# Performance work log

Hardware: AMD Instinct MI355X
Metric: run time of the kernel (lower is better)

The kernel has to match this reference:

```python
import jax, jax.numpy as jnp
import numpy as np

# Model dims (from init_kwargs + mamba_ssm defaults)
D_MODEL = 1024
N_LAYER = 2
D_STATE = 16
D_CONV = 4
D_INNER = 2 * D_MODEL          # expand=2
DT_RANK = D_MODEL // 16        # 64
VOCAB = 32000
BATCH, SEQLEN = 2, 1024


def setup_inputs() -> dict:
    key = jax.random.key(0)
    ks = jax.random.split(key, 10)
    s = 0.02
    x = jax.random.randint(ks[0], (BATCH, SEQLEN), 0, VOCAB)
    embedding = jax.random.normal(ks[1], (VOCAB, D_MODEL), dtype=jnp.float32) * s
    norm_w = jnp.ones((N_LAYER, D_MODEL), dtype=jnp.float32)
    in_proj_w = jax.random.normal(ks[2], (N_LAYER, 2 * D_INNER, D_MODEL), dtype=jnp.float32) * s
    conv_w = jax.random.normal(ks[3], (N_LAYER, D_INNER, D_CONV), dtype=jnp.float32) * (1.0 / np.sqrt(D_CONV))
    conv_b = jnp.zeros((N_LAYER, D_INNER), dtype=jnp.float32)
    x_proj_w = jax.random.normal(ks[4], (N_LAYER, DT_RANK + 2 * D_STATE, D_INNER), dtype=jnp.float32) * s
    dt_proj_w = jax.random.normal(ks[5], (N_LAYER, D_INNER, DT_RANK), dtype=jnp.float32) * (DT_RANK ** -0.5)
    # inverse-softplus of dt_init ~ 0.01 (mamba default dt range)
    dt_bias = jnp.full((N_LAYER, D_INNER), float(np.log(np.expm1(0.01))), dtype=jnp.float32)
    A_log = jnp.log(jnp.broadcast_to(jnp.arange(1, D_STATE + 1, dtype=jnp.float32), (N_LAYER, D_INNER, D_STATE)))
    D = jnp.ones((N_LAYER, D_INNER), dtype=jnp.float32)
    out_proj_w = jax.random.normal(ks[6], (N_LAYER, D_MODEL, D_INNER), dtype=jnp.float32) * s
    final_norm_w = jnp.ones((D_MODEL,), dtype=jnp.float32)
    return {"x": x, "embedding": embedding, "norm_w": norm_w, "in_proj_w": in_proj_w,
            "conv_w": conv_w, "conv_b": conv_b, "x_proj_w": x_proj_w, "dt_proj_w": dt_proj_w,
            "dt_bias": dt_bias, "A_log": A_log, "D": D, "out_proj_w": out_proj_w,
            "final_norm_w": final_norm_w}


def _rmsnorm(h, w, eps=1e-5):
    return h * jax.lax.rsqrt(jnp.mean(h * h, axis=-1, keepdims=True) + eps) * w


def _scan_combine(c1, c2):
    a1, b1 = c1
    a2, b2 = c2
    return a2 * a1, a2 * b1 + b2


def _mamba_block(h, norm_w, in_proj_w, conv_w, conv_b, x_proj_w, dt_proj_w, dt_bias, A_log, D, out_proj_w):
    u = _rmsnorm(h, norm_w)
    xz = jnp.einsum('bld,ed->ble', u, in_proj_w)           # [B,L,2*D_INNER]
    xi, z = jnp.split(xz, 2, axis=-1)
    # depthwise causal conv1d, kernel D_CONV
    k = conv_w.T[:, None, :]                               # [D_CONV, 1, D_INNER]
    xc = jax.lax.conv_general_dilated(xi, k, (1,), [(D_CONV - 1, 0)],
                                      dimension_numbers=('NLC', 'LIO', 'NLC'),
                                      feature_group_count=D_INNER) + conv_b
    xc = jax.nn.silu(xc)
    dbl = jnp.einsum('bld,ed->ble', xc, x_proj_w)          # [B,L,DT_RANK+2*D_STATE]
    dt_low = dbl[..., :DT_RANK]
    Bm = dbl[..., DT_RANK:DT_RANK + D_STATE]
    Cm = dbl[..., DT_RANK + D_STATE:]
    dt = jax.nn.softplus(jnp.einsum('blr,dr->bld', dt_low, dt_proj_w) + dt_bias)
    A = -jnp.exp(A_log)                                    # [D_INNER, D_STATE]
    a = jnp.exp(dt[..., None] * A)                         # [B,L,D_INNER,D_STATE]
    b = dt[..., None] * Bm[:, :, None, :] * xc[..., None]  # [B,L,D_INNER,D_STATE]
    hs = jax.lax.associative_scan(_scan_combine, (a, b), axis=1)[1]
    y = jnp.einsum('bldn,bln->bld', hs, Cm) + xc * D
    y = y * jax.nn.silu(z)
    return h + jnp.einsum('bld,md->blm', y, out_proj_w)


def reference(x, embedding, norm_w, in_proj_w, conv_w, conv_b, x_proj_w, dt_proj_w,
              dt_bias, A_log, D, out_proj_w, final_norm_w):
    h = embedding[x]                                       # [B,L,D_MODEL]
    for i in range(N_LAYER):
        h = _mamba_block(h, norm_w[i], in_proj_w[i], conv_w[i], conv_b[i], x_proj_w[i],
                         dt_proj_w[i], dt_bias[i], A_log[i], D[i], out_proj_w[i])
    h = _rmsnorm(h, final_norm_w)
    logits = jnp.einsum('bld,vd->blv', h, embedding)       # tied lm head
    return logits
```

## Files before the change

### kernel.cpp

```cpp
#include <hip/hip_runtime.h>
#include <hip/hip_bf16.h>
#include <math.h>

#define D_MODEL 1024
#define N_LAYER 2
#define D_STATE 16
#define D_CONV  4
#define D_INNER 2048
#define DT_RANK 64
#define VOCAB   32000
#define BATCH   2
#define SEQLEN  1024
#define TOKENS  (BATCH*SEQLEN)
#define NC      32
#define CL      32

typedef __hip_bfloat16 bf16;
typedef __bf16 bf16x8 __attribute__((ext_vector_type(8)));
typedef float f32x4 __attribute__((ext_vector_type(4)));

__device__ inline void gld_lds16(const bf16* g, bf16* l) {
    __builtin_amdgcn_global_load_lds(
        (const __attribute__((address_space(1))) void*)g,
        (__attribute__((address_space(3))) void*)l, 16, 0, 0);
}

__device__ inline float softplus_fast(float v) {
    return (v > 20.f) ? v : __logf(1.f + __expf(v));
}
__device__ inline float silu_fast(float v) {
    return v / (1.f + __expf(-v));
}

__global__ __launch_bounds__(256) void embed_kernel(const int* __restrict__ x,
                                                    const float* __restrict__ emb,
                                                    float* __restrict__ h) {
    int t = blockIdx.x;
    int tok = x[t];
    const float4* src = (const float4*)(emb + (size_t)tok * D_MODEL);
    float4* dst = (float4*)(h + (size_t)t * D_MODEL);
    dst[threadIdx.x] = src[threadIdx.x];
}

__global__ __launch_bounds__(256) void rmsnorm_bf16(const float* __restrict__ h,
                                                    const float* __restrict__ w,
                                                    bf16* __restrict__ u) {
    int t = blockIdx.x;
    const float4* hv = (const float4*)(h + (size_t)t * D_MODEL);
    float4 v = hv[threadIdx.x];
    float ss = v.x*v.x + v.y*v.y + v.z*v.z + v.w*v.w;
    #pragma unroll
    for (int off = 32; off > 0; off >>= 1) ss += __shfl_down(ss, off);
    __shared__ float red[4];
    int lane = threadIdx.x & 63, wid = threadIdx.x >> 6;
    if (lane == 0) red[wid] = ss;
    __syncthreads();
    float tot = red[0] + red[1] + red[2] + red[3];
    float scale = rsqrtf(tot * (1.0f / (float)D_MODEL) + 1e-5f);
    float4 wq = ((const float4*)w)[threadIdx.x];
    size_t o = (size_t)t * D_MODEL + threadIdx.x * 4;
    u[o+0] = __float2bfloat16(v.x * scale * wq.x);
    u[o+1] = __float2bfloat16(v.y * scale * wq.y);
    u[o+2] = __float2bfloat16(v.z * scale * wq.z);
    u[o+3] = __float2bfloat16(v.w * scale * wq.w);
}

__global__ __launch_bounds__(256) void f32_to_bf16(const float* __restrict__ s,
                                                   bf16* __restrict__ d, int n) {
    int i = (blockIdx.x * 256 + threadIdx.x) * 4;
    if (i < n) {
        float4 v = *(const float4*)(s + i);
        d[i+0] = __float2bfloat16(v.x);
        d[i+1] = __float2bfloat16(v.y);
        d[i+2] = __float2bfloat16(v.z);
        d[i+3] = __float2bfloat16(v.w);
    }
}

__global__ __launch_bounds__(256) void conv_xproj_pad(const float* __restrict__ s,
                                                      bf16* __restrict__ d) {
    int col = blockIdx.x * 256 + threadIdx.x;
    int row = blockIdx.y;
    int layer = blockIdx.z;
    float v = (row < 96) ? s[((size_t)layer * 96 + row) * D_INNER + col] : 0.f;
    d[((size_t)layer * 128 + row) * D_INNER + col] = __float2bfloat16(v);
}

__global__ __launch_bounds__(256) void gemm_bf16(
    const bf16* __restrict__ A, int lda,
    const bf16* __restrict__ W, int ldw,
    float* __restrict__ C, int ldc,
    int N, int K, int acc, int swz, int M, int bfout)
{
    __shared__ bf16 lds[2][2][128 * 64];
    int bx = blockIdx.x, by = blockIdx.y;
    if (swz) {
        int bid = by * gridDim.x + bx;
        int q = (gridDim.x * gridDim.y) >> 3;
        int n = (bid & 7) * q + (bid >> 3);
        by = n % gridDim.y;
        bx = n / gridDim.y;
    }
    const int z = blockIdx.z;
    A += (size_t)z * K;
    W += (size_t)z * K;
    C += (size_t)z * M * (size_t)ldc;

    const int tid  = threadIdx.x;
    const int wave = tid >> 6;
    const int lane = tid & 63;
    const int wr = wave >> 1, wc = wave & 1;
    const size_t rowBase = (size_t)by * 128;
    const size_t colBase = (size_t)bx * 128;

    const int srow = 8 * wave + (lane >> 3);
    const int scol = ((lane & 7) ^ (lane >> 3)) << 3;
    const bf16* aGs = A + (rowBase + srow) * (size_t)lda + scol;
    const bf16* bGs = W + (colBase + srow) * (size_t)ldw + scol;

#define STAGE(tt, bb) do {                                                      \
        const size_t kofs_ = (size_t)(tt) * 64;                                 \
        _Pragma("unroll")                                                       \
        for (int i_ = 0; i_ < 4; ++i_) {                                        \
            gld_lds16(aGs + kofs_ + (size_t)(32 * i_) * lda,                    \
                      &lds[bb][0][(32 * i_ + 8 * wave) * 64]);                  \
            gld_lds16(bGs + kofs_ + (size_t)(32 * i_) * ldw,                    \
                      &lds[bb][1][(32 * i_ + 8 * wave) * 64]);                  \
        }                                                                       \
    } while (0)

    f32x4 accv[4][4];
    #pragma unroll
    for (int i = 0; i < 4; ++i)
        #pragma unroll
        for (int j = 0; j < 4; ++j)
            accv[i][j] = f32x4{0.f, 0.f, 0.f, 0.f};

    const int arow0 = wr * 64 + (lane & 15);
    const int brow0 = wc * 64 + (lane & 15);
    const int h8  = (lane >> 4) << 3;
    const int sw8 = (lane & 7) << 3;

    const int NT = K >> 6;
    STAGE(0, 0);
    for (int t = 0; t < NT; ++t) {
        const int cur = t & 1;
        if (t + 1 < NT) {
            STAGE(t + 1, cur ^ 1);
            asm volatile("s_waitcnt vmcnt(8)" ::: "memory");
        } else {
            asm volatile("s_waitcnt vmcnt(0)" ::: "memory");
        }
        __builtin_amdgcn_s_barrier();

        const bf16* Ab = &lds[cur][0][0];
        const bf16* Bb = &lds[cur][1][0];
        #pragma unroll
        for (int kk = 0; kk < 2; ++kk) {
            const int cs = ((kk << 5) + h8) ^ sw8;
            bf16x8 af[4], bv[4];
            #pragma unroll
            for (int i = 0; i < 4; ++i)
                af[i] = *(const bf16x8*)(Ab + (arow0 + 16 * i) * 64 + cs);
            #pragma unroll
            for (int j = 0; j < 4; ++j)
                bv[j] = *(const bf16x8*)(Bb + (brow0 + 16 * j) * 64 + cs);
            #pragma unroll
            for (int i = 0; i < 4; ++i)
                #pragma unroll
                for (int j = 0; j < 4; ++j)
                    accv[i][j] = __builtin_amdgcn_mfma_f32_16x16x32_bf16(
                        af[i], bv[j], accv[i][j], 0, 0, 0);
        }
        asm volatile("s_waitcnt lgkmcnt(0)" ::: "memory");
        __builtin_amdgcn_s_barrier();
    }
#undef STAGE

    const int cl = lane & 15;
    const int rg = (lane >> 4) * 4;
    #pragma unroll
    for (int i = 0; i < 4; ++i) {
        #pragma unroll
        for (int j = 0; j < 4; ++j) {
            int col = (int)colBase + wc * 64 + j * 16 + cl;
            if (col < N) {
                size_t base = (rowBase + wr * 64 + i * 16 + rg) * (size_t)ldc + col;
                if (bfout) {
                    bf16* Cb = (bf16*)C;
                    #pragma unroll
                    for (int r = 0; r < 4; ++r)
                        Cb[base + (size_t)r * ldc] = __float2bfloat16(accv[i][j][r]);
                } else {
                    #pragma unroll
                    for (int r = 0; r < 4; ++r) {
                        size_t idx = base + (size_t)r * ldc;
                        C[idx] = acc ? C[idx] + accv[i][j][r] : accv[i][j][r];
                    }
                }
            }
        }
    }
}

__global__ __launch_bounds__(512) void gemm_wide3(
    const bf16* __restrict__ A,
    const bf16* __restrict__ W,
    float* __restrict__ C, int ldc, int bfout)
{
    __shared__ bf16 ldsA[3][256 * 32];
    __shared__ bf16 ldsB[3][128 * 32];
    int bx = blockIdx.x, by = blockIdx.y;
    {
        int bid = by * gridDim.x + bx;
        int n = (bid & 7) * ((gridDim.x * gridDim.y) >> 3) + (bid >> 3);
        by = n & 7;
        bx = n >> 3;
    }
    const int tid  = threadIdx.x;
    const int wave = tid >> 6;
    const int lane = tid & 63;
    const int wr = wave >> 1;
    const int wc = wave & 1;
    const size_t rowBase = (size_t)by * 256;
    const size_t colBase = (size_t)bx * 128;

    const int srow   = lane >> 2;
    const int schunk = ((lane & 3) ^ ((lane >> 3) & 3)) << 3;
    const bf16* aG0 = A + (rowBase + 16 * wave       + srow) * (size_t)D_MODEL + schunk;
    const bf16* aG1 = A + (rowBase + 128 + 16 * wave + srow) * (size_t)D_MODEL + schunk;
    const bf16* bG  = W + (colBase + 16 * wave       + srow) * (size_t)D_MODEL + schunk;

#define STAGEW(tt, sAp, sBp) do {                                               \
        const size_t ko_ = (size_t)(tt) * 32;                                   \
        gld_lds16(aG0 + ko_, (sAp) + 512 * wave);                               \
        gld_lds16(aG1 + ko_, (sAp) + 512 * (8 + wave));                         \
        gld_lds16(bG  + ko_, (sBp) + 512 * wave);                               \
    } while (0)

    f32x4 accv[4][4];
    #pragma unroll
    for (int i = 0; i < 4; ++i)
        #pragma unroll
        for (int j = 0; j < 4; ++j)
            accv[i][j] = f32x4{0.f, 0.f, 0.f, 0.f};

    const int l15 = lane & 15;
    const int cs = (((lane >> 4) ^ ((l15 >> 1) & 3)) << 3);
    const int arow0 = wr * 64 + l15;
    const int brow0 = wc * 64 + l15;

    STAGEW(0, &ldsA[0][0], &ldsB[0][0]);
    STAGEW(1, &ldsA[1][0], &ldsB[1][0]);

    int rs = 0, ps = 2;
    #pragma unroll 1
    for (int t = 0; t < 32; ++t) {
        if (t < 31) { asm volatile("s_waitcnt vmcnt(3)" ::: "memory"); }
        else        { asm volatile("s_waitcnt vmcnt(0)" ::: "memory"); }
        __builtin_amdgcn_s_barrier();
        __builtin_amdgcn_sched_barrier(0);

        if (t + 2 < 32) STAGEW(t + 2, &ldsA[ps][0], &ldsB[ps][0]);

        const bf16* Ab = &ldsA[rs][0];
        const bf16* Bb = &ldsB[rs][0];
        bf16x8 af[4], bv[4];
        #pragma unroll
        for (int i = 0; i < 4; ++i)
            af[i] = *(const bf16x8*)(Ab + (arow0 + 16 * i) * 32 + cs);
        #pragma unroll
        for (int j = 0; j < 4; ++j)
            bv[j] = *(const bf16x8*)(Bb + (brow0 + 16 * j) * 32 + cs);
        #pragma unroll
        for (int i = 0; i < 4; ++i)
            #pragma unroll
            for (int j = 0; j < 4; ++j)
                accv[i][j] = __builtin_amdgcn_mfma_f32_16x16x32_bf16(
                    af[i], bv[j], accv[i][j], 0, 0, 0);

        rs = (rs == 2) ? 0 : rs + 1;
        ps = (ps == 2) ? 0 : ps + 1;
    }
#undef STAGEW

    const int cl = l15;
    const int rg = (lane >> 4) * 4;
    #pragma unroll
    for (int i = 0; i < 4; ++i) {
        #pragma unroll
        for (int j = 0; j < 4; ++j) {
            int col = (int)colBase + wc * 64 + j * 16 + cl;
            size_t base = (rowBase + wr * 64 + i * 16 + rg) * (size_t)ldc + col;
            if (bfout) {
                bf16* Cb = (bf16*)C;
                #pragma unroll
                for (int r = 0; r < 4; ++r)
                    Cb[base + (size_t)r * ldc] = __float2bfloat16(accv[i][j][r]);
            } else {
                #pragma unroll
                for (int r = 0; r < 4; ++r)
                    C[base + (size_t)r * ldc] = accv[i][j][r];
            }
        }
    }
}

__global__ __launch_bounds__(256) void conv_silu_kernel(const bf16* __restrict__ xz,
                                                        const float* __restrict__ cw,
                                                        const float* __restrict__ cb,
                                                        bf16* __restrict__ xcb) {
    int d = blockIdx.x * 256 + threadIdx.x;
    int l0 = blockIdx.y * 8;
    int b = blockIdx.z;
    float w0 = cw[d*4+0], w1 = cw[d*4+1], w2 = cw[d*4+2], w3 = cw[d*4+3];
    float bias = cb[d];
    float win0 = (l0 >= 3) ? __bfloat162float(xz[((size_t)b * SEQLEN + l0 - 3) * (2*D_INNER) + d]) : 0.f;
    float win1 = (l0 >= 2) ? __bfloat162float(xz[((size_t)b * SEQLEN + l0 - 2) * (2*D_INNER) + d]) : 0.f;
    float win2 = (l0 >= 1) ? __bfloat162float(xz[((size_t)b * SEQLEN + l0 - 1) * (2*D_INNER) + d]) : 0.f;
    #pragma unroll
    for (int i = 0; i < 8; ++i) {
        float cur = __bfloat162float(xz[((size_t)b * SEQLEN + l0 + i) * (2*D_INNER) + d]);
        float acc = bias + w0*win0 + w1*win1 + w2*win2 + w3*cur;
        float s = silu_fast(acc);
        xcb[((size_t)b * SEQLEN + l0 + i) * D_INNER + d] = __float2bfloat16(s);
        win0 = win1; win1 = win2; win2 = cur;
    }
}

__global__ __launch_bounds__(256) void reduce_xproj(const float* __restrict__ px,
                                                    float* __restrict__ dblf,
                                                    bf16* __restrict__ dbl_b) {
    int i = blockIdx.x * 256 + threadIdx.x;
    float s = 0.f;
    #pragma unroll
    for (int z = 0; z < 8; ++z) s += px[(size_t)z * (TOKENS*96) + i];
    dblf[i] = s;
    dbl_b[i] = __float2bfloat16(s);
}

__global__ __launch_bounds__(256) void reduce_oproj(const float* __restrict__ po,
                                                    float* __restrict__ h) {
    int i = (blockIdx.x * 256 + threadIdx.x) * 4;
    float4 a = *(const float4*)(po + i);
    float4 b = *(const float4*)(po + (size_t)TOKENS*D_MODEL + i);
    float4 hv = *(const float4*)(h + i);
    hv.x += a.x + b.x; hv.y += a.y + b.y; hv.z += a.z + b.z; hv.w += a.w + b.w;
    *(float4*)(h + i) = hv;
}

__global__ __launch_bounds__(256) void scan_chunk(const bf16* __restrict__ dtp,
                                                  const float* __restrict__ dt_bias,
                                                  const float* __restrict__ dbl,
                                                  const bf16* __restrict__ xc,
                                                  const float* __restrict__ A_log,
                                                  float* __restrict__ aprod,
                                                  float* __restrict__ sfin) {
    int d = blockIdx.x * 256 + threadIdx.x;
    int c = blockIdx.y;
    int b = blockIdx.z;
    __shared__ float Bs[CL][D_STATE];
    for (int i = threadIdx.x; i < CL * D_STATE; i += 256) {
        int l = i >> 4, n = i & 15;
        Bs[l][n] = dbl[((size_t)b * SEQLEN + c * CL + l) * 96 + DT_RANK + n];
    }
    __syncthreads();
    float A[D_STATE];
    #pragma unroll
    for (int n = 0; n < D_STATE; ++n) A[n] = -__expf(A_log[d * D_STATE + n]);
    float bias = dt_bias[d];
    float st[D_STATE];
    #pragma unroll
    for (int n = 0; n < D_STATE; ++n) st[n] = 0.f;
    float dts = 0.f;
    for (int l = 0; l < CL; ++l) {
        size_t t = (size_t)b * SEQLEN + c * CL + l;
        float dtv = softplus_fast(__bfloat162float(dtp[t * D_INNER + d]) + bias);
        dts += dtv;
        float dx = dtv * __bfloat162float(xc[t * D_INNER + d]);
        #pragma unroll
        for (int n = 0; n < D_STATE; ++n) {
            float a = __expf(dtv * A[n]);
            st[n] = a * st[n] + dx * Bs[l][n];
        }
    }
    #pragma unroll
    for (int n = 0; n < D_STATE; ++n) {
        size_t o = (((size_t)b * NC + c) * D_STATE + n) * D_INNER + d;
        aprod[o] = __expf(dts * A[n]);
        sfin[o] = st[n];
    }
}

__global__ __launch_bounds__(256) void scan_carry(const float* __restrict__ aprod,
                                                  const float* __restrict__ sfin,
                                                  float* __restrict__ initS) {
    int idx = blockIdx.x * 256 + threadIdx.x;
    int d = idx & (D_INNER - 1);
    int n = (idx >> 11) & (D_STATE - 1);
    int b = idx >> 15;
    float st = 0.f;
    for (int c = 0; c < NC; ++c) {
        size_t o = (((size_t)b * NC + c) * D_STATE + n) * D_INNER + d;
        initS[o] = st;
        st = aprod[o] * st + sfin[o];
    }
}

__global__ __launch_bounds__(256) void scan_emit(const bf16* __restrict__ dtp,
                                                 const float* __restrict__ dt_bias,
                                                 const float* __restrict__ dbl,
                                                 const bf16* __restrict__ xc,
                                                 const bf16* __restrict__ xz,
                                                 const float* __restrict__ A_log,
                                                 const float* __restrict__ Dp,
                                                 const float* __restrict__ initS,
                                                 bf16* __restrict__ y) {
    int d = blockIdx.x * 256 + threadIdx.x;
    int c = blockIdx.y;
    int b = blockIdx.z;
    __shared__ float BCs[CL][2 * D_STATE];
    for (int i = threadIdx.x; i < CL * 2 * D_STATE; i += 256) {
        int l = i >> 5, n = i & 31;
        BCs[l][n] = dbl[((size_t)b * SEQLEN + c * CL + l) * 96 + DT_RANK + n];
    }
    __syncthreads();
    float A[D_STATE];
    #pragma unroll
    for (int n = 0; n < D_STATE; ++n) A[n] = -__expf(A_log[d * D_STATE + n]);
    float bias = dt_bias[d];
    float Dv = Dp[d];
    float st[D_STATE];
    #pragma unroll
    for (int n = 0; n < D_STATE; ++n)
        st[n] = initS[(((size_t)b * NC + c) * D_STATE + n) * D_INNER + d];
    for (int l = 0; l < CL; ++l) {
        size_t t = (size_t)b * SEQLEN + c * CL + l;
        float dtv = softplus_fast(__bfloat162float(dtp[t * D_INNER + d]) + bias);
        float xcv = __bfloat162float(xc[t * D_INNER + d]);
        float dx = dtv * xcv;
        float acc = 0.f;
        #pragma unroll
        for (int n = 0; n < D_STATE; ++n) {
            float a = __expf(dtv * A[n]);
            st[n] = a * st[n] + dx * BCs[l][n];
            acc += st[n] * BCs[l][D_STATE + n];
        }
        acc += xcv * Dv;
        float zv = __bfloat162float(xz[t * (2 * D_INNER) + D_INNER + d]);
        y[t * D_INNER + d] = __float2bfloat16(acc * silu_fast(zv));
    }
}

extern "C" void kernel_launch(void* const* d_in, const int* in_sizes, int n_in,
                              void* d_out, int out_size, void* d_ws, size_t ws_size,
                              hipStream_t stream) {
    const int*   x          = (const int*)  d_in[0];
    const float* emb        = (const float*)d_in[1];
    const float* norm_w     = (const float*)d_in[2];
    const float* in_proj_w  = (const float*)d_in[3];
    const float* conv_w     = (const float*)d_in[4];
    const float* conv_b     = (const float*)d_in[5];
    const float* x_proj_w   = (const float*)d_in[6];
    const float* dt_proj_w  = (const float*)d_in[7];
    const float* dt_bias    = (const float*)d_in[8];
    const float* A_log      = (const float*)d_in[9];
    const float* Dp         = (const float*)d_in[10];
    const float* out_proj_w = (const float*)d_in[11];
    const float* fnorm_w    = (const float*)d_in[12];
    float* out = (float*)d_out;
    float* ws  = (float*)d_ws;

    bf16*  embf   = (bf16*)ws;
    bf16*  u_b    = (bf16*)(ws + 16384000);
    bf16*  xz_b   = (bf16*)(ws + 17432576);
    bf16*  dtp_b  = (bf16*)(ws + 25821184);
    bf16*  xc_b   = (bf16*)(ws + 30015488);
    float* h      = ws + 36306944;
    float* dblf   = ws + 38404096;
    bf16*  dbl_b  = (bf16*)(ws + 38600704);
    bf16*  y_b    = (bf16*)(ws + 38699008);
    bf16*  inpj_b = (bf16*)(ws + 40796160);
    bf16*  xpj_b  = (bf16*)(ws + 44990464);
    bf16*  dtpj_b = (bf16*)(ws + 45252608);
    bf16*  otpj_b = (bf16*)(ws + 45383680);
    float* aprod  = ws + 47480832;
    float* sfin   = ws + 49577984;
    float* initS  = ws + 51675136;
    float* px     = ws + 53772288;
    float* po     = ws + 55345152;

    f32_to_bf16<<<(VOCAB*D_MODEL/4 + 255)/256, 256, 0, stream>>>(emb, embf, VOCAB*D_MODEL);
    f32_to_bf16<<<(2*2*D_INNER*D_MODEL/4 + 255)/256, 256, 0, stream>>>(in_proj_w,  inpj_b, 2*2*D_INNER*D_MODEL);
    conv_xproj_pad<<<dim3(D_INNER/256, 128, N_LAYER), 256, 0, stream>>>(x_proj_w, xpj_b);
    f32_to_bf16<<<(2*D_INNER*DT_RANK/4 + 255)/256, 256, 0, stream>>>(dt_proj_w,  dtpj_b, 2*D_INNER*DT_RANK);
    f32_to_bf16<<<(2*D_MODEL*D_INNER/4 + 255)/256, 256, 0, stream>>>(out_proj_w, otpj_b, 2*D_MODEL*D_INNER);

    embed_kernel<<<TOKENS, 256, 0, stream>>>(x, emb, h);

    for (int layer = 0; layer < N_LAYER; ++layer) {
        rmsnorm_bf16<<<TOKENS, 256, 0, stream>>>(h, norm_w + layer * D_MODEL, u_b);
        gemm_wide3<<<dim3(4096/128, TOKENS/256), 512, 0, stream>>>(
            u_b, inpj_b + (size_t)layer * 2 * D_INNER * D_MODEL,
            (float*)xz_b, 2 * D_INNER, 1);
        conv_silu_kernel<<<dim3(D_INNER/256, SEQLEN/8, BATCH), 256, 0, stream>>>(
            xz_b, conv_w + (size_t)layer * D_INNER * D_CONV, conv_b + layer * D_INNER,
            xc_b);
        gemm_bf16<<<dim3(1, TOKENS/128, 8), 256, 0, stream>>>(
            xc_b, D_INNER, xpj_b + (size_t)layer * 128 * D_INNER, D_INNER,
            px, 96, 96, 256, 0, 0, TOKENS, 0);
        reduce_xproj<<<(TOKENS*96)/256, 256, 0, stream>>>(px, dblf, dbl_b);
        gemm_bf16<<<dim3(D_INNER/128, TOKENS/128), 256, 0, stream>>>(
            dbl_b, 96, dtpj_b + (size_t)layer * D_INNER * DT_RANK, DT_RANK,
            (float*)dtp_b, D_INNER, D_INNER, DT_RANK, 0, 1, TOKENS, 1);
        scan_chunk<<<dim3(D_INNER/256, NC, BATCH), 256, 0, stream>>>(
            dtp_b, dt_bias + layer * D_INNER, dblf, xc_b,
            A_log + (size_t)layer * D_INNER * D_STATE, aprod, sfin);
        scan_carry<<<(BATCH*D_STATE*D_INNER)/256, 256, 0, stream>>>(aprod, sfin, initS);
        scan_emit<<<dim3(D_INNER/256, NC, BATCH), 256, 0, stream>>>(
            dtp_b, dt_bias + layer * D_INNER, dblf, xc_b, xz_b,
            A_log + (size_t)layer * D_INNER * D_STATE, Dp + layer * D_INNER,
            initS, y_b);
        gemm_bf16<<<dim3(D_MODEL/128, TOKENS/128, 2), 256, 0, stream>>>(
            y_b, D_INNER, otpj_b + (size_t)layer * D_MODEL * D_INNER, D_INNER,
            po, D_MODEL, D_MODEL, 1024, 0, 1, TOKENS, 0);
        reduce_oproj<<<(TOKENS*D_MODEL/4)/256, 256, 0, stream>>>(po, h);
    }

    rmsnorm_bf16<<<TOKENS, 256, 0, stream>>>(h, fnorm_w, u_b);

    gemm_wide3<<<dim3(VOCAB/128, TOKENS/256), 512, 0, stream>>>(u_b, embf, out, VOCAB, 0);
}
```

Before: 545.5 us.

## Add dedicated 256x128 vocab GEMM and fuse residual reduce with RMSNorm

Replaces the final LM-head GEMM with a specialized kernel that uses 256 threads per 256x128 tile, so each wave owns a 128x64 sub-tile. It uses triple-buffered LDS staging via direct global-to-LDS loads and a grouped block swizzle for L2 reuse of the embedding weights. It also fuses the out-proj partial-sum reduction with the next layer's RMSNorm (or the final norm), which removes separate rmsnorm launches and an extra pass over h. The larger per-wave accumulator tile raises register pressure and may lower occupancy.

```diff
diff --git a/kernel.cpp b/kernel.cpp
--- a/kernel.cpp
+++ b/kernel.cpp
@@ -306,6 +306,104 @@
     }
 }
 
+__global__ __launch_bounds__(256) void gemm_vocab4(
+    const bf16* __restrict__ A,
+    const bf16* __restrict__ W,
+    float* __restrict__ C)
+{
+    __shared__ bf16 ldsA[3][256 * 32];
+    __shared__ bf16 ldsB[3][128 * 32];
+    int bx = blockIdx.x, by = blockIdx.y;
+    {
+        int bid = by * gridDim.x + bx;
+        int n = (bid & 7) * ((gridDim.x * gridDim.y) >> 3) + (bid >> 3);
+        by = n & 7;
+        bx = n >> 3;
+    }
+    const int tid  = threadIdx.x;
+    const int wave = tid >> 6;
+    const int lane = tid & 63;
+    const int wr = wave >> 1;
+    const int wc = wave & 1;
+    const size_t rowBase = (size_t)by * 256;
+    const size_t colBase = (size_t)bx * 128;
+
+    const int srow   = lane >> 2;
+    const int schunk = ((lane & 3) ^ ((lane >> 3) & 3)) << 3;
+    const bf16* aG = A + (rowBase + 64 * wave + srow) * (size_t)D_MODEL + schunk;
+    const bf16* bG = W + (colBase + 32 * wave + srow) * (size_t)D_MODEL + schunk;
+
+#define STGV(tt, sl) do {                                                       \
+        const size_t ko_ = (size_t)(tt) * 32;                                   \
+        gld_lds16(aG + ko_,                          &ldsA[sl][(64*wave     )*32]); \
+        gld_lds16(aG + ko_ + (size_t)16 * D_MODEL,   &ldsA[sl][(64*wave + 16)*32]); \
+        gld_lds16(aG + ko_ + (size_t)32 * D_MODEL,   &ldsA[sl][(64*wave + 32)*32]); \
+        gld_lds16(aG + ko_ + (size_t)48 * D_MODEL,   &ldsA[sl][(64*wave + 48)*32]); \
+        gld_lds16(bG + ko_,                          &ldsB[sl][(32*wave     )*32]); \
+        gld_lds16(bG + ko_ + (size_t)16 * D_MODEL,   &ldsB[sl][(32*wave + 16)*32]); \
+    } while (0)
+
+    f32x4 accv[8][4];
+    #pragma unroll
+    for (int i = 0; i < 8; ++i)
+        #pragma unroll
+        for (int j = 0; j < 4; ++j)
+            accv[i][j] = f32x4{0.f, 0.f, 0.f, 0.f};
+
+    const int l15 = lane & 15;
+    const int cs = (((lane >> 4) ^ ((l15 >> 1) & 3)) << 3);
+    const int arow0 = wr * 128 + l15;
+    const int brow0 = wc * 64 + l15;
+
+    STGV(0, 0);
+    STGV(1, 1);
+
+    int rs = 0, ps = 2;
+    #pragma unroll 1
+    for (int t = 0; t < 32; ++t) {
+        if (t < 31) { asm volatile("s_waitcnt vmcnt(6)" ::: "memory"); }
+        else        { asm volatile("s_waitcnt vmcnt(0)" ::: "memory"); }
+        __builtin_amdgcn_s_barrier();
+        __builtin_amdgcn_sched_barrier(0);
+
+        if (t + 2 < 32) STGV(t + 2, ps);
+
+        const bf16* Ab = &ldsA[rs][0];
+        const bf16* Bb = &ldsB[rs][0];
+        bf16x8 af[8], bv[4];
+        #pragma unroll
+        for (int j = 0; j < 4; ++j)
+            bv[j] = *(const bf16x8*)(Bb + (brow0 + 16 * j) * 32 + cs);
+        #pragma unroll
+        for (int i = 0; i < 8; ++i)
+            af[i] = *(const bf16x8*)(Ab + (arow0 + 16 * i) * 32 + cs);
+        #pragma unroll
+        for (int i = 0; i < 8; ++i)
+            #pragma unroll
+            for (int j = 0; j < 4; ++j)
+                accv[i][j] = __builtin_amdgcn_mfma_f32_16x16x32_bf16(
+                    af[i], bv[j], accv[i][j], 0, 0, 0);
+
+        rs = (rs == 2) ? 0 : rs + 1;
+        ps = (ps == 2) ? 0 : ps + 1;
+    }
+#undef STGV
+
+    const int cl = l15;
+    const int rg = (lane >> 4) * 4;
+    #pragma unroll
+    for (int i = 0; i < 8; ++i) {
+        #pragma unroll
+        for (int j = 0; j < 4; ++j) {
+            int col = (int)colBase + wc * 64 + j * 16 + cl;
+            size_t base = (rowBase + wr * 128 + i * 16 + rg) * (size_t)VOCAB + col;
+            #pragma unroll
+            for (int r = 0; r < 4; ++r)
+                C[base + (size_t)r * VOCAB] = accv[i][j][r];
+        }
+    }
+}
+
 __global__ __launch_bounds__(256) void conv_silu_kernel(const bf16* __restrict__ xz,
                                                         const float* __restrict__ cw,
                                                         const float* __restrict__ cb,
@@ -339,14 +437,31 @@
     dbl_b[i] = __float2bfloat16(s);
 }
 
-__global__ __launch_bounds__(256) void reduce_oproj(const float* __restrict__ po,
-                                                    float* __restrict__ h) {
-    int i = (blockIdx.x * 256 + threadIdx.x) * 4;
-    float4 a = *(const float4*)(po + i);
-    float4 b = *(const float4*)(po + (size_t)TOKENS*D_MODEL + i);
-    float4 hv = *(const float4*)(h + i);
+__global__ __launch_bounds__(256) void reduce_oproj_rms(const float* __restrict__ po,
+                                                        float* __restrict__ h,
+                                                        const float* __restrict__ w,
+                                                        bf16* __restrict__ u) {
+    int t = blockIdx.x;
+    size_t base = (size_t)t * D_MODEL + threadIdx.x * 4;
+    float4 a = *(const float4*)(po + base);
+    float4 b = *(const float4*)(po + (size_t)TOKENS * D_MODEL + base);
+    float4 hv = *(const float4*)(h + base);
     hv.x += a.x + b.x; hv.y += a.y + b.y; hv.z += a.z + b.z; hv.w += a.w + b.w;
-    *(float4*)(h + i) = hv;
+    *(float4*)(h + base) = hv;
+    float ss = hv.x*hv.x + hv.y*hv.y + hv.z*hv.z + hv.w*hv.w;
+    #pragma unroll
+    for (int off = 32; off > 0; off >>= 1) ss += __shfl_down(ss, off);
+    __shared__ float red[4];
+    int lane = threadIdx.x & 63, wid = threadIdx.x >> 6;
+    if (lane == 0) red[wid] = ss;
+    __syncthreads();
+    float tot = red[0] + red[1] + red[2] + red[3];
+    float scale = rsqrtf(tot * (1.0f / (float)D_MODEL) + 1e-5f);
+    float4 wq = ((const float4*)w)[threadIdx.x];
+    u[base+0] = __float2bfloat16(hv.x * scale * wq.x);
+    u[base+1] = __float2bfloat16(hv.y * scale * wq.y);
+    u[base+2] = __float2bfloat16(hv.z * scale * wq.z);
+    u[base+3] = __float2bfloat16(hv.w * scale * wq.w);
 }
 
 __global__ __launch_bounds__(256) void scan_chunk(const bf16* __restrict__ dtp,
@@ -497,9 +612,9 @@
     f32_to_bf16<<<(2*D_MODEL*D_INNER/4 + 255)/256, 256, 0, stream>>>(out_proj_w, otpj_b, 2*D_MODEL*D_INNER);
 
     embed_kernel<<<TOKENS, 256, 0, stream>>>(x, emb, h);
+    rmsnorm_bf16<<<TOKENS, 256, 0, stream>>>(h, norm_w, u_b);
 
     for (int layer = 0; layer < N_LAYER; ++layer) {
-        rmsnorm_bf16<<<TOKENS, 256, 0, stream>>>(h, norm_w + layer * D_MODEL, u_b);
         gemm_wide3<<<dim3(4096/128, TOKENS/256), 512, 0, stream>>>(
             u_b, inpj_b + (size_t)layer * 2 * D_INNER * D_MODEL,
             (float*)xz_b, 2 * D_INNER, 1);
@@ -524,10 +639,10 @@
         gemm_bf16<<<dim3(D_MODEL/128, TOKENS/128, 2), 256, 0, stream>>>(
             y_b, D_INNER, otpj_b + (size_t)layer * D_MODEL * D_INNER, D_INNER,
             po, D_MODEL, D_MODEL, 1024, 0, 1, TOKENS, 0);
-        reduce_oproj<<<(TOKENS*D_MODEL/4)/256, 256, 0, stream>>>(po, h);
-    }
-
-    rmsnorm_bf16<<<TOKENS, 256, 0, stream>>>(h, fnorm_w, u_b);
-
-    gemm_wide3<<<dim3(VOCAB/128, TOKENS/256), 512, 0, stream>>>(u_b, embf, out, VOCAB, 0);
-}
+        reduce_oproj_rms<<<TOKENS, 256, 0, stream>>>(
+            po, h, (layer + 1 < N_LAYER) ? (norm_w + (layer + 1) * D_MODEL) : fnorm_w,
+            u_b);
+    }
+
+    gemm_vocab4<<<dim3(VOCAB/128, TOKENS/256), 256, 0, stream>>>(u_b, embf, out);
+}
```

New measurement: 550.4 us. No clear change (+0.9%).

## Fuse rmsnorm into embed and out-proj reduce, bf16 partials, recompute scan decay

Applied to the files above, without the earlier changes.

Merges the embedding gather with the first RMSNorm, and the out-projection split-K reduction with the next layer's (or the final) RMSNorm. This removes three rmsnorm launches and their re-reads of h. The out-projection split-K partials are now written as bf16 instead of fp32, halving that traffic but rounding the partial sums. The scan's per-chunk decay products are no longer stored per state; only the per-channel dt sum is written and scan_carry recomputes exp(dts*A), cutting memory traffic in exchange for extra exp work.

```diff
diff --git a/kernel.cpp b/kernel.cpp
--- a/kernel.cpp
+++ b/kernel.cpp
@@ -31,23 +31,22 @@
 __device__ inline float silu_fast(float v) {
     return v / (1.f + __expf(-v));
 }
-
-__global__ __launch_bounds__(256) void embed_kernel(const int* __restrict__ x,
-                                                    const float* __restrict__ emb,
-                                                    float* __restrict__ h) {
+__device__ inline float bfu(unsigned short s) {
+    unsigned u = ((unsigned)s) << 16;
+    float f;
+    __builtin_memcpy(&f, &u, 4);
+    return f;
+}
+
+__global__ __launch_bounds__(256) void embed_rms(const int* __restrict__ x,
+                                                 const float* __restrict__ emb,
+                                                 const float* __restrict__ w,
+                                                 float* __restrict__ h,
+                                                 bf16* __restrict__ u) {
     int t = blockIdx.x;
     int tok = x[t];
-    const float4* src = (const float4*)(emb + (size_t)tok * D_MODEL);
-    float4* dst = (float4*)(h + (size_t)t * D_MODEL);
-    dst[threadIdx.x] = src[threadIdx.x];
-}
-
-__global__ __launch_bounds__(256) void rmsnorm_bf16(const float* __restrict__ h,
-                                                    const float* __restrict__ w,
-                                                    bf16* __restrict__ u) {
-    int t = blockIdx.x;
-    const float4* hv = (const float4*)(h + (size_t)t * D_MODEL);
-    float4 v = hv[threadIdx.x];
+    float4 v = ((const float4*)(emb + (size_t)tok * D_MODEL))[threadIdx.x];
+    ((float4*)(h + (size_t)t * D_MODEL))[threadIdx.x] = v;
     float ss = v.x*v.x + v.y*v.y + v.z*v.z + v.w*v.w;
     #pragma unroll
     for (int off = 32; off > 0; off >>= 1) ss += __shfl_down(ss, off);
@@ -104,7 +103,8 @@
     const int z = blockIdx.z;
     A += (size_t)z * K;
     W += (size_t)z * K;
-    C += (size_t)z * M * (size_t)ldc;
+    float* Cf = C + (size_t)z * M * (size_t)ldc;
+    bf16*  Cb = (bf16*)C + (size_t)z * M * (size_t)ldc;
 
     const int tid  = threadIdx.x;
     const int wave = tid >> 6;
@@ -187,7 +187,6 @@
             if (col < N) {
                 size_t base = (rowBase + wr * 64 + i * 16 + rg) * (size_t)ldc + col;
                 if (bfout) {
-                    bf16* Cb = (bf16*)C;
                     #pragma unroll
                     for (int r = 0; r < 4; ++r)
                         Cb[base + (size_t)r * ldc] = __float2bfloat16(accv[i][j][r]);
@@ -195,7 +194,7 @@
                     #pragma unroll
                     for (int r = 0; r < 4; ++r) {
                         size_t idx = base + (size_t)r * ldc;
-                        C[idx] = acc ? C[idx] + accv[i][j][r] : accv[i][j][r];
+                        Cf[idx] = acc ? Cf[idx] + accv[i][j][r] : accv[i][j][r];
                     }
                 }
             }
@@ -339,14 +338,34 @@
     dbl_b[i] = __float2bfloat16(s);
 }
 
-__global__ __launch_bounds__(256) void reduce_oproj(const float* __restrict__ po,
-                                                    float* __restrict__ h) {
-    int i = (blockIdx.x * 256 + threadIdx.x) * 4;
-    float4 a = *(const float4*)(po + i);
-    float4 b = *(const float4*)(po + (size_t)TOKENS*D_MODEL + i);
-    float4 hv = *(const float4*)(h + i);
-    hv.x += a.x + b.x; hv.y += a.y + b.y; hv.z += a.z + b.z; hv.w += a.w + b.w;
-    *(float4*)(h + i) = hv;
+__global__ __launch_bounds__(256) void reduce_oproj_rms(const bf16* __restrict__ po,
+                                                        float* __restrict__ h,
+                                                        const float* __restrict__ w,
+                                                        bf16* __restrict__ u) {
+    int t = blockIdx.x;
+    size_t base = (size_t)t * D_MODEL + threadIdx.x * 4;
+    ushort4 ua = *(const ushort4*)(po + base);
+    ushort4 ub = *(const ushort4*)(po + (size_t)TOKENS * D_MODEL + base);
+    float4 hv = *(const float4*)(h + base);
+    hv.x += bfu(ua.x) + bfu(ub.x);
+    hv.y += bfu(ua.y) + bfu(ub.y);
+    hv.z += bfu(ua.z) + bfu(ub.z);
+    hv.w += bfu(ua.w) + bfu(ub.w);
+    *(float4*)(h + base) = hv;
+    float ss = hv.x*hv.x + hv.y*hv.y + hv.z*hv.z + hv.w*hv.w;
+    #pragma unroll
+    for (int off = 32; off > 0; off >>= 1) ss += __shfl_down(ss, off);
+    __shared__ float red[4];
+    int lane = threadIdx.x & 63, wid = threadIdx.x >> 6;
+    if (lane == 0) red[wid] = ss;
+    __syncthreads();
+    float tot = red[0] + red[1] + red[2] + red[3];
+    float scale = rsqrtf(tot * (1.0f / (float)D_MODEL) + 1e-5f);
+    float4 wq = ((const float4*)w)[threadIdx.x];
+    u[base+0] = __float2bfloat16(hv.x * scale * wq.x);
+    u[base+1] = __float2bfloat16(hv.y * scale * wq.y);
+    u[base+2] = __float2bfloat16(hv.z * scale * wq.z);
+    u[base+3] = __float2bfloat16(hv.w * scale * wq.w);
 }
 
 __global__ __launch_bounds__(256) void scan_chunk(const bf16* __restrict__ dtp,
@@ -354,7 +373,7 @@
                                                   const float* __restrict__ dbl,
                                                   const bf16* __restrict__ xc,
                                                   const float* __restrict__ A_log,
-                                                  float* __restrict__ aprod,
+                                                  float* __restrict__ dts_out,
                                                   float* __restrict__ sfin) {
     int d = blockIdx.x * 256 + threadIdx.x;
     int c = blockIdx.y;
@@ -384,26 +403,29 @@
             st[n] = a * st[n] + dx * Bs[l][n];
         }
     }
+    dts_out[((size_t)b * NC + c) * D_INNER + d] = dts;
     #pragma unroll
     for (int n = 0; n < D_STATE; ++n) {
         size_t o = (((size_t)b * NC + c) * D_STATE + n) * D_INNER + d;
-        aprod[o] = __expf(dts * A[n]);
         sfin[o] = st[n];
     }
 }
 
-__global__ __launch_bounds__(256) void scan_carry(const float* __restrict__ aprod,
+__global__ __launch_bounds__(256) void scan_carry(const float* __restrict__ dts,
                                                   const float* __restrict__ sfin,
+                                                  const float* __restrict__ A_log,
                                                   float* __restrict__ initS) {
     int idx = blockIdx.x * 256 + threadIdx.x;
     int d = idx & (D_INNER - 1);
     int n = (idx >> 11) & (D_STATE - 1);
     int b = idx >> 15;
+    float A = -__expf(A_log[d * D_STATE + n]);
     float st = 0.f;
     for (int c = 0; c < NC; ++c) {
         size_t o = (((size_t)b * NC + c) * D_STATE + n) * D_INNER + d;
         initS[o] = st;
-        st = aprod[o] * st + sfin[o];
+        float ap = __expf(dts[((size_t)b * NC + c) * D_INNER + d] * A);
+        st = ap * st + sfin[o];
     }
 }
 
@@ -484,11 +506,11 @@
     bf16*  xpj_b  = (bf16*)(ws + 44990464);
     bf16*  dtpj_b = (bf16*)(ws + 45252608);
     bf16*  otpj_b = (bf16*)(ws + 45383680);
-    float* aprod  = ws + 47480832;
+    float* dts    = ws + 47480832;
     float* sfin   = ws + 49577984;
     float* initS  = ws + 51675136;
     float* px     = ws + 53772288;
-    float* po     = ws + 55345152;
+    bf16*  po_b   = (bf16*)(ws + 55345152);
 
     f32_to_bf16<<<(VOCAB*D_MODEL/4 + 255)/256, 256, 0, stream>>>(emb, embf, VOCAB*D_MODEL);
     f32_to_bf16<<<(2*2*D_INNER*D_MODEL/4 + 255)/256, 256, 0, stream>>>(in_proj_w,  inpj_b, 2*2*D_INNER*D_MODEL);
@@ -496,10 +518,9 @@
     f32_to_bf16<<<(2*D_INNER*DT_RANK/4 + 255)/256, 256, 0, stream>>>(dt_proj_w,  dtpj_b, 2*D_INNER*DT_RANK);
     f32_to_bf16<<<(2*D_MODEL*D_INNER/4 + 255)/256, 256, 0, stream>>>(out_proj_w, otpj_b, 2*D_MODEL*D_INNER);
 
-    embed_kernel<<<TOKENS, 256, 0, stream>>>(x, emb, h);
+    embed_rms<<<TOKENS, 256, 0, stream>>>(x, emb, norm_w, h, u_b);
 
     for (int layer = 0; layer < N_LAYER; ++layer) {
-        rmsnorm_bf16<<<TOKENS, 256, 0, stream>>>(h, norm_w + layer * D_MODEL, u_b);
         gemm_wide3<<<dim3(4096/128, TOKENS/256), 512, 0, stream>>>(
             u_b, inpj_b + (size_t)layer * 2 * D_INNER * D_MODEL,
             (float*)xz_b, 2 * D_INNER, 1);
@@ -515,19 +536,20 @@
             (float*)dtp_b, D_INNER, D_INNER, DT_RANK, 0, 1, TOKENS, 1);
         scan_chunk<<<dim3(D_INNER/256, NC, BATCH), 256, 0, stream>>>(
             dtp_b, dt_bias + layer * D_INNER, dblf, xc_b,
-            A_log + (size_t)layer * D_INNER * D_STATE, aprod, sfin);
-        scan_carry<<<(BATCH*D_STATE*D_INNER)/256, 256, 0, stream>>>(aprod, sfin, initS);
+            A_log + (size_t)layer * D_INNER * D_STATE, dts, sfin);
+        scan_carry<<<(BATCH*D_STATE*D_INNER)/256, 256, 0, stream>>>(
+            dts, sfin, A_log + (size_t)layer * D_INNER * D_STATE, initS);
         scan_emit<<<dim3(D_INNER/256, NC, BATCH), 256, 0, stream>>>(
             dtp_b, dt_bias + layer * D_INNER, dblf, xc_b, xz_b,
             A_log + (size_t)layer * D_INNER * D_STATE, Dp + layer * D_INNER,
             initS, y_b);
         gemm_bf16<<<dim3(D_MODEL/128, TOKENS/128, 2), 256, 0, stream>>>(
             y_b, D_INNER, otpj_b + (size_t)layer * D_MODEL * D_INNER, D_INNER,
-            po, D_MODEL, D_MODEL, 1024, 0, 1, TOKENS, 0);
-        reduce_oproj<<<(TOKENS*D_MODEL/4)/256, 256, 0, stream>>>(po, h);
-    }
-
-    rmsnorm_bf16<<<TOKENS, 256, 0, stream>>>(h, fnorm_w, u_b);
+            (float*)po_b, D_MODEL, D_MODEL, 1024, 0, 1, TOKENS, 1);
+        reduce_oproj_rms<<<TOKENS, 256, 0, stream>>>(
+            po_b, h, (layer + 1 < N_LAYER) ? (norm_w + (layer + 1) * D_MODEL) : fnorm_w,
+            u_b);
+    }
 
     gemm_wide3<<<dim3(VOCAB/128, TOKENS/256), 512, 0, stream>>>(u_b, embf, out, VOCAB, 0);
 }
```

Result: faster. 531.2 us (-2.6%).
